# Performance work log

Measured on AMD Instinct MI355X. Metric: run time of the kernel, lower is better.

## Reference

```python
import jax, jax.numpy as jnp
import numpy as np

# Matches init_kwargs: pc_range=[-54,-54,-5,54,54,3], voxel_size=[0.2,0.2,1.0]
PC_LO = jnp.array([-54.0, -54.0, -5.0], jnp.float32)
PC_HI = jnp.array([54.0, 54.0, 3.0], jnp.float32)
VOX = jnp.array([0.2, 0.2, 1.0], jnp.float32)
NX, NY, NZ = 540, 540, 8          # round((hi-lo)/voxel_size), x,y,z order
NV = NX * NY * NZ                  # dense voxel count (2,332,800)


def setup_inputs() -> dict:
    key = jax.random.key(0)
    B, N = 4, 300000
    k1, k2 = jax.random.split(key)
    center = (PC_LO + PC_HI) / 2.0
    half = (PC_HI - PC_LO) / 2.0 * 1.05
    xyz = center + (jax.random.uniform(k1, (B, N, 3), jnp.float32) * 2.0 - 1.0) * half
    feats = jax.random.normal(k2, (B, N, 2), jnp.float32)
    points = jnp.concatenate([xyz, feats], axis=-1)  # [B, N, 5]
    return {"points": points}


def reference(points):
    """Dynamic voxelization: range filter + quantize + scatter-mean per voxel.

    torch's data-dependent `unique` + compaction is not jit-shapeable, so the
    per-voxel means are returned on the dense [NV, F] grid (occupied voxels are
    those with counts > 0); the math per occupied voxel is identical to the
    original scatter_mean over unique coords.
    """
    grid_max = jnp.array([NX - 1, NY - 1, NZ - 1], jnp.int32)

    def voxelize(pts):  # pts: [N, 5]
        xyz = pts[:, :3]
        keep = jnp.all((xyz >= PC_LO) & (xyz <= PC_HI), axis=1)  # [N]
        # coords in (z, y, x) order in the original; compute (x,y,z) then linearize as z-major
        c = jnp.floor((xyz - PC_LO) / VOX).astype(jnp.int32)
        c = jnp.clip(c, 0, grid_max)  # boundary points (x == hi) map to last cell
        lin = (c[:, 2] * NY + c[:, 1]) * NX + c[:, 0]  # [N]
        lin = jnp.where(keep, lin, NV)  # dropped points -> dummy segment
        pts_m = jnp.where(keep[:, None], pts, 0.0)
        sums = jax.ops.segment_sum(pts_m, lin, num_segments=NV + 1)[:NV]            # [NV, 5]
        cnts = jax.ops.segment_sum(keep.astype(pts.dtype), lin, num_segments=NV + 1)[:NV]  # [NV]
        means = sums / jnp.maximum(cnts, 1.0)[:, None]
        return means, cnts

    voxels, counts = jax.vmap(voxelize)(points)  # [B, NV, 5], [B, NV]
    shape_np = jnp.array([NX, NY, NZ], jnp.int32)
    return voxels, counts, shape_np
```

## Files before the change

kernel.cpp:

```cpp
#include <hip/hip_runtime.h>


#define NX_ 540
#define NY_ 540
#define NZ_ 8
#define NV_ (NX_ * NY_ * NZ_)
#define B_ 4
#define N_ 300000
#define BN_ (B_ * N_)
#define NVB_ (B_ * NV_)



__global__ __launch_bounds__(256) void voxel_build(
    const float* __restrict__ pts,
    int* __restrict__ head,
    float* __restrict__ nodes)
{
    int g = blockIdx.x * blockDim.x + threadIdx.x;
    if (g >= BN_) return;

    const float* p = pts + (size_t)g * 5;
    float x  = p[0];
    float y  = p[1];
    float z  = p[2];
    float f0 = p[3];
    float f1 = p[4];

    bool keep = (x >= -54.0f) & (x <= 54.0f) &
                (y >= -54.0f) & (y <= 54.0f) &
                (z >= -5.0f)  & (z <= 3.0f);
    if (!keep) return;

    int cx = (int)floorf((x + 54.0f) * 5.0f);
    int cy = (int)floorf((y + 54.0f) * 5.0f);
    int cz = (int)floorf(z + 5.0f);
    cx = min(max(cx, 0), NX_ - 1);
    cy = min(max(cy, 0), NY_ - 1);
    cz = min(max(cz, 0), NZ_ - 1);

    int lin = (cz * NY_ + cy) * NX_ + cx;
    int b = g / N_;
    int vox = b * NV_ + lin;

    float* nb = nodes + (size_t)g * 8;
    *(float4*)nb = make_float4(x, y, z, f0);

    int old = atomicExch(&head[vox], g);

    float2 tail;
    tail.x = f1;
    tail.y = __int_as_float(old);
    *(float2*)(nb + 4) = tail;
}

__global__ __launch_bounds__(256) void voxel_output(
    const int* __restrict__ head,
    const float* __restrict__ nodes,
    float* __restrict__ means,
    float* __restrict__ cnts,
    float* __restrict__ shape_out)
{
    int v = blockIdx.x * blockDim.x + threadIdx.x;
    if (v == 0) {
        shape_out[0] = 540.0f;
        shape_out[1] = 540.0f;
        shape_out[2] = 8.0f;
    }
    if (v >= NVB_) return;

    int i = head[v];
    float s0 = 0.f, s1 = 0.f, s2 = 0.f, s3 = 0.f, s4 = 0.f;
    int c = 0;
    while (i >= 0) {
        const float* nb = nodes + (size_t)i * 8;
        float4 a = *(const float4*)nb;
        float2 t = *(const float2*)(nb + 4);
        s0 += a.x; s1 += a.y; s2 += a.z; s3 += a.w; s4 += t.x;
        c++;
        i = __float_as_int(t.y);
    }

    float d = (float)max(c, 1);
    size_t mb = (size_t)v * 5;
    means[mb + 0] = s0 / d;
    means[mb + 1] = s1 / d;
    means[mb + 2] = s2 / d;
    means[mb + 3] = s3 / d;
    means[mb + 4] = s4 / d;
    cnts[v] = (float)c;
}


__global__ __launch_bounds__(256) void voxel_scatter(
    const float* __restrict__ pts,
    float* __restrict__ sums,
    float* __restrict__ cnts)
{
    int g = blockIdx.x * blockDim.x + threadIdx.x;
    if (g >= BN_) return;
    const float* p = pts + (size_t)g * 5;
    float x = p[0], y = p[1], z = p[2], f0 = p[3], f1 = p[4];
    bool keep = (x >= -54.0f) & (x <= 54.0f) &
                (y >= -54.0f) & (y <= 54.0f) &
                (z >= -5.0f)  & (z <= 3.0f);
    if (!keep) return;
    int cx = (int)floorf((x + 54.0f) * 5.0f);
    int cy = (int)floorf((y + 54.0f) * 5.0f);
    int cz = (int)floorf(z + 5.0f);
    cx = min(max(cx, 0), NX_ - 1);
    cy = min(max(cy, 0), NY_ - 1);
    cz = min(max(cz, 0), NZ_ - 1);
    int lin = (cz * NY_ + cy) * NX_ + cx;
    int b = g / N_;
    size_t vox = (size_t)b * NV_ + (size_t)lin;
    size_t base = vox * 5;
    atomicAdd(&sums[base + 0], x);
    atomicAdd(&sums[base + 1], y);
    atomicAdd(&sums[base + 2], z);
    atomicAdd(&sums[base + 3], f0);
    atomicAdd(&sums[base + 4], f1);
    atomicAdd(&cnts[vox], 1.0f);
}

__global__ __launch_bounds__(256) void voxel_finalize(
    float* __restrict__ sums,
    const float* __restrict__ cnts,
    float* __restrict__ shape_out)
{
    size_t idx = (size_t)blockIdx.x * blockDim.x + threadIdx.x;
    if (idx == 0) {
        shape_out[0] = 540.0f;
        shape_out[1] = 540.0f;
        shape_out[2] = 8.0f;
    }
    if (idx >= (size_t)NVB_) return;
    float c = cnts[idx];
    if (c > 0.0f) {
        size_t base = idx * 5;
        sums[base + 0] /= c;
        sums[base + 1] /= c;
        sums[base + 2] /= c;
        sums[base + 3] /= c;
        sums[base + 4] /= c;
    }
}


extern "C" void kernel_launch(void* const* d_in, const int* in_sizes, int n_in,
                              void* d_out, int out_size, void* d_ws, size_t ws_size,
                              hipStream_t stream) {
    const float* points = (const float*)d_in[0];
    float* out = (float*)d_out;

    float* means     = out;
    float* cnts      = out + (size_t)NVB_ * 5;
    float* shape_out = out + (size_t)NVB_ * 6;

    const size_t head_bytes = (size_t)NVB_ * 4;
    const size_t node_bytes = (size_t)BN_ * 32;
    const size_t need = head_bytes + node_bytes;

    if (ws_size >= need) {
        int*   head  = (int*)d_ws;
        float* nodes = (float*)((char*)d_ws + head_bytes);

        hipMemsetAsync(head, 0xFF, head_bytes, stream);

        voxel_build<<<(BN_ + 255) / 256, 256, 0, stream>>>(points, head, nodes);
        voxel_output<<<(NVB_ + 255) / 256, 256, 0, stream>>>(head, nodes, means, cnts, shape_out);
    } else {
        hipMemsetAsync(d_out, 0, (size_t)out_size * sizeof(float), stream);
        voxel_scatter<<<(BN_ + 255) / 256, 256, 0, stream>>>(points, means, cnts);
        voxel_finalize<<<(NVB_ + 255) / 256, 256, 0, stream>>>(means, cnts, shape_out);
    }
}
```

Measured before the change: 329.2 us.

## Use index-only linked list and vectorized 4-voxel output writes

The build kernel now stores only a next-index per point instead of copying 32-byte nodes with the point data. The output kernel walks the list and gathers features straight from the original points array. Each thread also handles four consecutive voxels, using int4 head loads and float4 stores for means and counts. This removes the node write traffic and packs the dense output writes, at the cost of unaligned 5-float gathers from points and a serial loop over four voxels per thread.

```diff
diff --git a/kernel.cpp b/kernel.cpp
--- a/kernel.cpp
+++ b/kernel.cpp
@@ -11,21 +11,18 @@
 #define NVB_ (B_ * NV_)
 
 
-
 __global__ __launch_bounds__(256) void voxel_build(
     const float* __restrict__ pts,
     int* __restrict__ head,
-    float* __restrict__ nodes)
+    int* __restrict__ nxt)
 {
     int g = blockIdx.x * blockDim.x + threadIdx.x;
     if (g >= BN_) return;
 
     const float* p = pts + (size_t)g * 5;
-    float x  = p[0];
-    float y  = p[1];
-    float z  = p[2];
-    float f0 = p[3];
-    float f1 = p[4];
+    float x = p[0];
+    float y = p[1];
+    float z = p[2];
 
     bool keep = (x >= -54.0f) & (x <= 54.0f) &
                 (y >= -54.0f) & (y <= 54.0f) &
@@ -43,52 +40,60 @@
     int b = g / N_;
     int vox = b * NV_ + lin;
 
-    float* nb = nodes + (size_t)g * 8;
-    *(float4*)nb = make_float4(x, y, z, f0);
-
     int old = atomicExch(&head[vox], g);
-
-    float2 tail;
-    tail.x = f1;
-    tail.y = __int_as_float(old);
-    *(float2*)(nb + 4) = tail;
+    nxt[g] = old;
 }
 
-__global__ __launch_bounds__(256) void voxel_output(
+
+__global__ __launch_bounds__(256) void voxel_output4(
     const int* __restrict__ head,
-    const float* __restrict__ nodes,
+    const int* __restrict__ nxt,
+    const float* __restrict__ pts,
     float* __restrict__ means,
     float* __restrict__ cnts,
     float* __restrict__ shape_out)
 {
-    int v = blockIdx.x * blockDim.x + threadIdx.x;
-    if (v == 0) {
+    int t = blockIdx.x * blockDim.x + threadIdx.x;
+    if (t == 0) {
         shape_out[0] = 540.0f;
         shape_out[1] = 540.0f;
         shape_out[2] = 8.0f;
     }
-    if (v >= NVB_) return;
+    int v0 = t * 4;
+    if (v0 >= NVB_) return;
 
-    int i = head[v];
-    float s0 = 0.f, s1 = 0.f, s2 = 0.f, s3 = 0.f, s4 = 0.f;
-    int c = 0;
-    while (i >= 0) {
-        const float* nb = nodes + (size_t)i * 8;
-        float4 a = *(const float4*)nb;
-        float2 t = *(const float2*)(nb + 4);
-        s0 += a.x; s1 += a.y; s2 += a.z; s3 += a.w; s4 += t.x;
-        c++;
-        i = __float_as_int(t.y);
+    int4 h4 = *(const int4*)(head + v0);
+    int hh[4] = {h4.x, h4.y, h4.z, h4.w};
+
+    float o[20];
+    float cf[4];
+
+    #pragma unroll
+    for (int j = 0; j < 4; j++) {
+        int i = hh[j];
+        float s0 = 0.f, s1 = 0.f, s2 = 0.f, s3 = 0.f, s4 = 0.f;
+        int c = 0;
+        while (i >= 0) {
+            const float* p = pts + (size_t)i * 5;
+            s0 += p[0]; s1 += p[1]; s2 += p[2]; s3 += p[3]; s4 += p[4];
+            c++;
+            i = nxt[i];
+        }
+        float d = (float)max(c, 1);
+        o[j * 5 + 0] = s0 / d;
+        o[j * 5 + 1] = s1 / d;
+        o[j * 5 + 2] = s2 / d;
+        o[j * 5 + 3] = s3 / d;
+        o[j * 5 + 4] = s4 / d;
+        cf[j] = (float)c;
     }
 
-    float d = (float)max(c, 1);
-    size_t mb = (size_t)v * 5;
-    means[mb + 0] = s0 / d;
-    means[mb + 1] = s1 / d;
-    means[mb + 2] = s2 / d;
-    means[mb + 3] = s3 / d;
-    means[mb + 4] = s4 / d;
-    cnts[v] = (float)c;
+    float* mb = means + (size_t)v0 * 5;
+    #pragma unroll
+    for (int k = 0; k < 5; k++) {
+        *(float4*)(mb + k * 4) = make_float4(o[k*4+0], o[k*4+1], o[k*4+2], o[k*4+3]);
+    }
+    *(float4*)(cnts + v0) = make_float4(cf[0], cf[1], cf[2], cf[3]);
 }
 
 
@@ -158,17 +163,20 @@
     float* shape_out = out + (size_t)NVB_ * 6;
 
     const size_t head_bytes = (size_t)NVB_ * 4;
-    const size_t node_bytes = (size_t)BN_ * 32;
-    const size_t need = head_bytes + node_bytes;
+    const size_t nxt_bytes  = (size_t)BN_ * 4;
+    const size_t need = head_bytes + nxt_bytes;
 
     if (ws_size >= need) {
-        int*   head  = (int*)d_ws;
-        float* nodes = (float*)((char*)d_ws + head_bytes);
+        int* head = (int*)d_ws;
+        int* nxt  = (int*)((char*)d_ws + head_bytes);
 
         hipMemsetAsync(head, 0xFF, head_bytes, stream);
 
-        voxel_build<<<(BN_ + 255) / 256, 256, 0, stream>>>(points, head, nodes);
-        voxel_output<<<(NVB_ + 255) / 256, 256, 0, stream>>>(head, nodes, means, cnts, shape_out);
+        voxel_build<<<(BN_ + 255) / 256, 256, 0, stream>>>(points, head, nxt);
+
+        int threads = NVB_ / 4;
+        voxel_output4<<<(threads + 255) / 256, 256, 0, stream>>>(
+            head, nxt, points, means, cnts, shape_out);
     } else {
         hipMemsetAsync(d_out, 0, (size_t)out_size * sizeof(float), stream);
         voxel_scatter<<<(BN_ + 255) / 256, 256, 0, stream>>>(points, means, cnts);
```

New measurement: 333.0 us. No clear change (+1.2%).
